# Optimization experiments

Hardware: AMD Instinct MI355X
Metric: run time of the kernel (lower is better)

Reference implementation:

```python
import jax, jax.numpy as jnp
import numpy as np
import math

N_NODES = 50000
N_EDGES = 600000
EMBED_DIM = 128


def setup_inputs() -> dict:
    key = jax.random.key(0)
    k_emb, k_edge, k_w = jax.random.split(key, 3)
    emb = jax.random.normal(k_emb, (N_NODES, EMBED_DIM), dtype=jnp.float32) * 0.1
    edges = jax.random.randint(k_edge, (2, N_EDGES), 0, N_NODES, dtype=jnp.int64)
    std = 1.0 / math.sqrt(EMBED_DIM)
    # nn.Linear(2*embed_dim, embed_dim): weight [out, in]
    W = jax.random.uniform(k_w, (EMBED_DIM, 2 * EMBED_DIM), dtype=jnp.float32,
                           minval=-std, maxval=std)
    b = jnp.zeros((EMBED_DIM,), dtype=jnp.float32)
    gamma = jnp.ones((EMBED_DIM,), dtype=jnp.float32)
    beta = jnp.zeros((EMBED_DIM,), dtype=jnp.float32)
    return {"emb": emb, "edges": edges, "W": W, "b": b, "gamma": gamma, "beta": beta}


def reference(emb, edges, W, b, gamma, beta):
    bsz = emb.shape[0]
    row = edges[0]  # destination / output node per edge (spmm row index)
    col = edges[1]  # source node per edge (spmm col index)
    # edge attention logits: <emb[dst], emb[src]> per edge, then exp
    attn = jnp.exp(jnp.sum(emb[row] * emb[col], axis=-1))  # [E]
    # special_spmm with ones -> per-row sum of attention weights
    denom = jax.ops.segment_sum(attn, row, num_segments=bsz)  # [N]
    # special_spmm with emb -> exp-weighted scatter-add of source embeddings
    agg = jax.ops.segment_sum(attn[:, None] * emb[col], row, num_segments=bsz)  # [N, D]
    agg = agg / (denom[:, None] + 1e-20)
    # concat + linear
    x = jnp.concatenate([emb, agg], axis=-1) @ W.T + b  # [N, D]
    # layer norm (eps=1e-5, affine)
    mu = jnp.mean(x, axis=-1, keepdims=True)
    var = jnp.mean((x - mu) ** 2, axis=-1, keepdims=True)
    x = (x - mu) * jax.lax.rsqrt(var + 1e-5) * gamma + beta
    return x
```

## Files before the change

kernel.cpp:

```cpp
#include <hip/hip_runtime.h>
#include <math.h>

#define D 128
#define TWO_D 256
#define CAP 64
#define CCAP 3584
#define CHUNK 2048

typedef __bf16 v8bf __attribute__((ext_vector_type(8)));
typedef float  v4f  __attribute__((ext_vector_type(4)));
typedef unsigned short us4 __attribute__((ext_vector_type(4)));
typedef unsigned short v8us __attribute__((ext_vector_type(8)));

#define OFF_CNT      0u
#define OFF_COLBUF   200192u
#define OFF_CCNT     6600192u
#define OFF_COARSE   6601216u
#define OFF_WBF16    10271232u
#define OFF_EMBB     10336768u
#define WS_TIER_A    23136768u

__global__ __launch_bounds__(256) void k_cvt_bin(
    const float* __restrict__ emb, const float* __restrict__ W,
    const int* __restrict__ edges,
    __bf16* __restrict__ embb, __bf16* __restrict__ Wb,
    unsigned int* __restrict__ ccnt, unsigned int* __restrict__ coarse,
    int nEmb8, int nW8, int E, int binB, int NB)
{
    if ((int)blockIdx.x < binB) {
        __shared__ unsigned int hist[256];
        __shared__ unsigned int base[256];
        __shared__ unsigned int run[256];
        int tid = threadIdx.x;
        int e0  = blockIdx.x * CHUNK;
        hist[tid] = 0;
        run[tid]  = 0;
        __syncthreads();

        int rs[CHUNK / 256];
        #pragma unroll
        for (int k = 0; k < CHUNK / 256; ++k) {
            int e = e0 + k * 256 + tid;
            rs[k] = -1;
            if (e < E) {
                int r = edges[e];
                rs[k] = r;
                atomicAdd(&hist[r >> 8], 1u);
            }
        }
        __syncthreads();
        if (tid < NB) {
            unsigned h = hist[tid];
            base[tid] = h ? atomicAdd(&ccnt[tid], h) : 0u;
        }
        __syncthreads();
        #pragma unroll
        for (int k = 0; k < CHUNK / 256; ++k) {
            int e = e0 + k * 256 + tid;
            if (e < E) {
                int r = rs[k];
                int c = edges[E + e];
                int bk = r >> 8;
                unsigned lp = atomicAdd(&run[bk], 1u);
                unsigned slot = base[bk] + lp;
                if (slot < CCAP)
                    coarse[(size_t)bk * CCAP + slot] =
                        ((unsigned)(r & 255) << 16) | (unsigned)c;
            }
        }
    } else {
        int tid = ((int)blockIdx.x - binB) * 256 + threadIdx.x;
        if (tid < nEmb8 + nW8) {
            const float* src;
            __bf16* dst;
            if (tid < nEmb8) { src = emb + (size_t)tid * 8; dst = embb + (size_t)tid * 8; }
            else { int j = (tid - nEmb8) * 8; src = W + j; dst = Wb + j; }
            float4 f0 = *(const float4*)(src);
            float4 f1 = *(const float4*)(src + 4);
            v8bf v;
            v[0] = (__bf16)f0.x; v[1] = (__bf16)f0.y; v[2] = (__bf16)f0.z; v[3] = (__bf16)f0.w;
            v[4] = (__bf16)f1.x; v[5] = (__bf16)f1.y; v[6] = (__bf16)f1.z; v[7] = (__bf16)f1.w;
            *(v8bf*)dst = v;
        }
    }
}

__global__ __launch_bounds__(256) void k_fine(
    const unsigned int* __restrict__ coarse,
    const unsigned int* __restrict__ ccnt,
    int* __restrict__ cnt, unsigned short* __restrict__ colbuf, int N)
{
    __shared__ __align__(16) unsigned short ftile[256 * CAP];
    __shared__ unsigned int fcnt[256];
    int tid = threadIdx.x;
    int b   = blockIdx.x;
    int r0  = b << 8;
    fcnt[tid] = 0;
    __syncthreads();

    unsigned mc = ccnt[b];
    if (mc > CCAP) mc = CCAP;
    for (unsigned i = tid; i < mc; i += 256) {
        unsigned p = coarse[(size_t)b * CCAP + i];
        unsigned rlo = p >> 16;
        unsigned c   = p & 0xFFFFu;
        unsigned lp  = atomicAdd(&fcnt[rlo], 1u);
        if (lp < CAP) ftile[rlo * CAP + lp] = (unsigned short)c;
    }
    __syncthreads();

    int r = r0 + tid;
    if (r < N) {
        unsigned d = fcnt[tid];
        cnt[r] = (int)(d > CAP ? CAP : d);
    }
    #pragma unroll
    for (int j = 0; j < 8; ++j) {
        int g  = j * 256 + tid;
        int rr = r0 + (g >> 3);
        if (rr < N)
            *(v8us*)(colbuf + (size_t)rr * CAP + (g & 7) * 8) =
                *(const v8us*)(ftile + (g >> 3) * CAP + (g & 7) * 8);
    }
}

__global__ __launch_bounds__(256) void gcn_agg_b(
    const __bf16* __restrict__ embb,
    const unsigned short* __restrict__ colbuf,
    const int* __restrict__ cnt,
    __bf16* __restrict__ aggb,
    int N)
{
    int grp = threadIdx.x >> 4;
    int il  = threadIdx.x & 15;
    int n   = blockIdx.x * 16 + grp;
    if (n >= N) return;

    v8bf a8 = *(const v8bf*)(embb + (size_t)n * D + il * 8);
    float af[8];
    #pragma unroll
    for (int q = 0; q < 8; ++q) af[q] = (float)a8[q];

    float acc[8];
    #pragma unroll
    for (int q = 0; q < 8; ++q) acc[q] = 0.f;
    float den = 0.f;

    int deg = cnt[n];
    if (deg > CAP) deg = CAP;
    const unsigned short* row = colbuf + (size_t)n * CAP;

    int e = 0;
    for (; e + 3 < deg; e += 4) {
        us4 c4 = *(const us4*)(row + e);
        v8bf v0 = *(const v8bf*)(embb + (size_t)c4[0] * D + il * 8);
        v8bf v1 = *(const v8bf*)(embb + (size_t)c4[1] * D + il * 8);
        v8bf v2 = *(const v8bf*)(embb + (size_t)c4[2] * D + il * 8);
        v8bf v3 = *(const v8bf*)(embb + (size_t)c4[3] * D + il * 8);
        float vf0[8], vf1[8], vf2[8], vf3[8];
        float t0 = 0.f, t1 = 0.f, t2 = 0.f, t3 = 0.f;
        #pragma unroll
        for (int q = 0; q < 8; ++q) {
            vf0[q] = (float)v0[q]; t0 += af[q] * vf0[q];
            vf1[q] = (float)v1[q]; t1 += af[q] * vf1[q];
            vf2[q] = (float)v2[q]; t2 += af[q] * vf2[q];
            vf3[q] = (float)v3[q]; t3 += af[q] * vf3[q];
        }
        #pragma unroll
        for (int off = 1; off <= 8; off <<= 1) {
            t0 += __shfl_xor(t0, off, 16);
            t1 += __shfl_xor(t1, off, 16);
            t2 += __shfl_xor(t2, off, 16);
            t3 += __shfl_xor(t3, off, 16);
        }
        float w0 = __expf(t0), w1 = __expf(t1);
        float w2 = __expf(t2), w3 = __expf(t3);
        #pragma unroll
        for (int q = 0; q < 8; ++q)
            acc[q] += (w0 * vf0[q] + w1 * vf1[q]) + (w2 * vf2[q] + w3 * vf3[q]);
        den += (w0 + w1) + (w2 + w3);
    }
    for (; e < deg; ++e) {
        int c0 = row[e];
        v8bf v0 = *(const v8bf*)(embb + (size_t)c0 * D + il * 8);
        float vf0[8];
        float t0 = 0.f;
        #pragma unroll
        for (int q = 0; q < 8; ++q) {
            vf0[q] = (float)v0[q];
            t0 += af[q] * vf0[q];
        }
        #pragma unroll
        for (int off = 1; off <= 8; off <<= 1)
            t0 += __shfl_xor(t0, off, 16);
        float w0 = __expf(t0);
        #pragma unroll
        for (int q = 0; q < 8; ++q) acc[q] += w0 * vf0[q];
        den += w0;
    }
    float inv = 1.0f / (den + 1e-20f);
    v8bf r;
    #pragma unroll
    for (int q = 0; q < 8; ++q) r[q] = (__bf16)(acc[q] * inv);
    *(v8bf*)(aggb + (size_t)n * 256 + il * 8) = r;
}

__global__ __launch_bounds__(256) void gcn_node_b(
    const __bf16* __restrict__ embb,
    const __bf16* __restrict__ Wb,
    const float* __restrict__ bias,
    const float* __restrict__ gamma,
    const float* __restrict__ beta,
    float* __restrict__ out, int N)
{
    __shared__ __align__(16) __bf16 xt[64 * 256];

    int t    = threadIdx.x;
    int wave = t >> 6;
    int lane = t & 63;
    int n0   = blockIdx.x * 64;
    const __bf16* aggb = (const __bf16*)out;

    #pragma unroll
    for (int j = 0; j < 8; ++j) {
        int gf = j * 64 + lane;
        int ml = gf >> 5;
        int m  = wave * 16 + ml;
        int g  = gf & 31;
        int n  = n0 + m;
        v8bf v;
        if (n < N) {
            v = (g < 16) ? *(const v8bf*)(embb + (size_t)n * D + g * 8)
                         : *(const v8bf*)(aggb + (size_t)n * 256 + (g - 16) * 8);
        } else {
            #pragma unroll
            for (int q = 0; q < 8; ++q) v[q] = (__bf16)0.0f;
        }
        *(v8bf*)(xt + (m * 32 + (g ^ (m & 7))) * 8) = v;
    }

    int mrow = lane & 15;
    int quad = lane >> 4;
    int mloc = wave * 16 + mrow;

    v8bf a[8];
    #pragma unroll
    for (int kt = 0; kt < 8; ++kt) {
        int g = (kt * 4 + quad) ^ (mloc & 7);
        a[kt] = *(const v8bf*)(xt + (mloc * 32 + g) * 8);
    }

    float bi[8], gm[8], bt[8];
    #pragma unroll
    for (int ft = 0; ft < 8; ++ft) {
        int f = ft * 16 + mrow;
        bi[ft] = bias[f]; gm[ft] = gamma[f]; bt[ft] = beta[f];
    }

    v4f accf[8];
    #pragma unroll
    for (int ft = 0; ft < 8; ++ft)
        #pragma unroll
        for (int r = 0; r < 4; ++r) accf[ft][r] = 0.0f;

    #pragma unroll
    for (int kt = 0; kt < 8; ++kt) {
        #pragma unroll
        for (int ft = 0; ft < 8; ++ft) {
            v8bf b = *(const v8bf*)(Wb + (ft * 16 + mrow) * TWO_D + kt * 32 + quad * 8);
            accf[ft] = __builtin_amdgcn_mfma_f32_16x16x32_bf16(a[kt], b, accf[ft], 0, 0, 0);
        }
    }

    #pragma unroll
    for (int ft = 0; ft < 8; ++ft)
        #pragma unroll
        for (int r = 0; r < 4; ++r) accf[ft][r] += bi[ft];

    #pragma unroll
    for (int r = 0; r < 4; ++r) {
        float s = 0.f, s2 = 0.f;
        #pragma unroll
        for (int ft = 0; ft < 8; ++ft) {
            float x = accf[ft][r];
            s += x; s2 += x * x;
        }
        #pragma unroll
        for (int off = 1; off <= 8; off <<= 1) {
            s  += __shfl_xor(s,  off, 64);
            s2 += __shfl_xor(s2, off, 64);
        }
        float mu  = s * (1.0f / 128.0f);
        float var = s2 * (1.0f / 128.0f) - mu * mu;
        float ivn = rsqrtf(var + 1e-5f);
        int n = n0 + wave * 16 + quad * 4 + r;
        if (n < N) {
            #pragma unroll
            for (int ft = 0; ft < 8; ++ft) {
                int f = ft * 16 + mrow;
                out[(size_t)n * D + f] = (accf[ft][r] - mu) * ivn * gm[ft] + bt[ft];
            }
        }
    }
}

__global__ __launch_bounds__(256) void gcn_edge_attn(
    const float* __restrict__ emb, const int* __restrict__ edges,
    float* __restrict__ agg, float* __restrict__ denom, int E) {
    int e    = (int)((blockIdx.x * 256u + threadIdx.x) >> 6);
    int lane = threadIdx.x & 63;
    if (e >= E) return;
    int row = edges[e];
    int col = edges[E + e];
    const float2 a = *(const float2*)(emb + (size_t)row * D + lane * 2);
    const float2 c = *(const float2*)(emb + (size_t)col * D + lane * 2);
    float s = a.x * c.x + a.y * c.y;
    #pragma unroll
    for (int off = 32; off >= 1; off >>= 1) s += __shfl_xor(s, off, 64);
    float attn = expf(s);
    float* dst = agg + (size_t)row * D + lane * 2;
    unsafeAtomicAdd(dst,     attn * c.x);
    unsafeAtomicAdd(dst + 1, attn * c.y);
    if (lane == 0) unsafeAtomicAdd(denom + row, attn);
}

__global__ __launch_bounds__(256) void gcn_node_fallback(
    const float* __restrict__ emb, const float* __restrict__ W,
    const float* __restrict__ bias, const float* __restrict__ gamma,
    const float* __restrict__ beta, const float* __restrict__ denom,
    float* __restrict__ out, int N) {
    __shared__ float scat[2][TWO_D];
    __shared__ float sred[2][4];
    int tid  = threadIdx.x;
    int g    = tid >> 7;
    int o    = tid & 127;
    int lane = tid & 63;
    int wig  = (tid >> 6) & 1;
    for (int n0 = blockIdx.x * 2; n0 < N; n0 += gridDim.x * 2) {
        int n = n0 + g;
        bool act = (n < N);
        if (act) {
            float ev  = emb[(size_t)n * D + o];
            float inv = 1.0f / (denom[n] + 1e-20f);
            scat[g][o]     = ev;
            scat[g][D + o] = out[(size_t)n * D + o] * inv;
        }
        __syncthreads();
        float acc = 0.f;
        if (act) {
            const float4* wr = (const float4*)(W + (size_t)o * TWO_D);
            #pragma unroll 4
            for (int k4 = 0; k4 < TWO_D / 4; ++k4) {
                float4 w = wr[k4];
                float4 a = *(const float4*)(&scat[g][k4 * 4]);
                acc += w.x * a.x + w.y * a.y + w.z * a.z + w.w * a.w;
            }
            acc += bias[o];
        }
        float s = acc, s2 = acc * acc;
        #pragma unroll
        for (int off = 32; off >= 1; off >>= 1) {
            s  += __shfl_xor(s,  off, 64);
            s2 += __shfl_xor(s2, off, 64);
        }
        if (lane == 0) { sred[g][wig * 2] = s; sred[g][wig * 2 + 1] = s2; }
        __syncthreads();
        if (act) {
            float ts  = sred[g][0] + sred[g][2];
            float ts2 = sred[g][1] + sred[g][3];
            float mu  = ts * (1.0f / 128.0f);
            float var = ts2 * (1.0f / 128.0f) - mu * mu;
            float inv = rsqrtf(var + 1e-5f);
            out[(size_t)n * D + o] = (acc - mu) * inv * gamma[o] + beta[o];
        }
        __syncthreads();
    }
}

extern "C" void kernel_launch(void* const* d_in, const int* in_sizes, int n_in,
                              void* d_out, int out_size, void* d_ws, size_t ws_size,
                              hipStream_t stream) {
    const float* emb   = (const float*)d_in[0];
    const int*   edges = (const int*)  d_in[1];
    const float* W     = (const float*)d_in[2];
    const float* bias  = (const float*)d_in[3];
    const float* gamma = (const float*)d_in[4];
    const float* beta  = (const float*)d_in[5];
    float* out = (float*)d_out;

    int N = in_sizes[0] / D;
    int E = in_sizes[1] / 2;

    if (ws_size >= (size_t)WS_TIER_A) {
        char* ws = (char*)d_ws;
        int*            cnt    = (int*)            (ws + OFF_CNT);
        unsigned short* colbuf = (unsigned short*) (ws + OFF_COLBUF);
        unsigned int*   ccnt   = (unsigned int*)   (ws + OFF_CCNT);
        unsigned int*   coarse = (unsigned int*)   (ws + OFF_COARSE);
        __bf16*         Wb     = (__bf16*)         (ws + OFF_WBF16);
        __bf16*         embb   = (__bf16*)         (ws + OFF_EMBB);

        int nEmb8 = N * D / 8;
        int nW8   = D * TWO_D / 8;
        int cvtB  = (nEmb8 + nW8 + 255) / 256;
        int binB  = (E + CHUNK - 1) / CHUNK;
        int NB    = (N + 255) >> 8;

        hipMemsetAsync(ccnt, 0, 1024, stream);
        k_cvt_bin<<<binB + cvtB, 256, 0, stream>>>(
            emb, W, edges, embb, Wb, ccnt, coarse, nEmb8, nW8, E, binB, NB);
        k_fine   <<<NB, 256, 0, stream>>>(coarse, ccnt, cnt, colbuf, N);
        gcn_agg_b<<<(N + 15) / 16, 256, 0, stream>>>(embb, colbuf, cnt,
                                                     (__bf16*)out, N);
        gcn_node_b<<<(N + 63) / 64, 256, 0, stream>>>(embb, Wb, bias, gamma,
                                                      beta, out, N);
    } else {
        float* denom = (float*)d_ws;
        hipMemsetAsync(out,   0, (size_t)N * D * sizeof(float), stream);
        hipMemsetAsync(denom, 0, (size_t)N * sizeof(float), stream);
        gcn_edge_attn<<<(E + 3) / 4, 256, 0, stream>>>(emb, edges, out, denom, E);
        gcn_node_fallback<<<512, 256, 0, stream>>>(emb, W, bias, gamma, beta,
                                                   denom, out, N);
    }
}
```

Measured before the change: 170.2 us.

## Unroll gather loop to 8 edges and streamline binning pass

The aggregation loop now handles 8 neighbours per iteration, issuing eight embedding-row gathers before any use to raise memory-level parallelism, with a 4-edge and a scalar tail. The binning kernel packs each edge's local offset into the histogram atomic's return value, which removes the second shared-memory atomic pass and the run array. CHUNK doubles to 4096, so fewer blocks do the binning. The 8-way unroll raises register pressure and may lower occupancy, and the 12-bit packed offset relies on CHUNK staying at or below 4096.

```diff
diff --git a/kernel.cpp b/kernel.cpp
--- a/kernel.cpp
+++ b/kernel.cpp
@@ -5,7 +5,7 @@
 #define TWO_D 256
 #define CAP 64
 #define CCAP 3584
-#define CHUNK 2048
+#define CHUNK 4096
 
 typedef __bf16 v8bf __attribute__((ext_vector_type(8)));
 typedef float  v4f  __attribute__((ext_vector_type(4)));
@@ -30,22 +30,19 @@
     if ((int)blockIdx.x < binB) {
         __shared__ unsigned int hist[256];
         __shared__ unsigned int base[256];
-        __shared__ unsigned int run[256];
         int tid = threadIdx.x;
         int e0  = blockIdx.x * CHUNK;
         hist[tid] = 0;
-        run[tid]  = 0;
-        __syncthreads();
-
-        int rs[CHUNK / 256];
+        __syncthreads();
+
+        unsigned rs[CHUNK / 256];
         #pragma unroll
         for (int k = 0; k < CHUNK / 256; ++k) {
             int e = e0 + k * 256 + tid;
-            rs[k] = -1;
             if (e < E) {
-                int r = edges[e];
-                rs[k] = r;
-                atomicAdd(&hist[r >> 8], 1u);
+                unsigned r  = (unsigned)edges[e];
+                unsigned lp = atomicAdd(&hist[r >> 8], 1u);
+                rs[k] = (r << 12) | lp;
             }
         }
         __syncthreads();
@@ -58,14 +55,14 @@
         for (int k = 0; k < CHUNK / 256; ++k) {
             int e = e0 + k * 256 + tid;
             if (e < E) {
-                int r = rs[k];
-                int c = edges[E + e];
+                unsigned pk = rs[k];
+                unsigned r  = pk >> 12;
+                unsigned lp = pk & 0xFFFu;
+                unsigned c  = (unsigned)edges[E + e];
                 int bk = r >> 8;
-                unsigned lp = atomicAdd(&run[bk], 1u);
                 unsigned slot = base[bk] + lp;
                 if (slot < CCAP)
-                    coarse[(size_t)bk * CCAP + slot] =
-                        ((unsigned)(r & 255) << 16) | (unsigned)c;
+                    coarse[(size_t)bk * CCAP + slot] = ((r & 255u) << 16) | c;
             }
         }
     } else {
@@ -151,20 +148,28 @@
     const unsigned short* row = colbuf + (size_t)n * CAP;
 
     int e = 0;
-    for (; e + 3 < deg; e += 4) {
-        us4 c4 = *(const us4*)(row + e);
-        v8bf v0 = *(const v8bf*)(embb + (size_t)c4[0] * D + il * 8);
-        v8bf v1 = *(const v8bf*)(embb + (size_t)c4[1] * D + il * 8);
-        v8bf v2 = *(const v8bf*)(embb + (size_t)c4[2] * D + il * 8);
-        v8bf v3 = *(const v8bf*)(embb + (size_t)c4[3] * D + il * 8);
-        float vf0[8], vf1[8], vf2[8], vf3[8];
+    for (; e + 7 < deg; e += 8) {
+        v8us c8 = *(const v8us*)(row + e);
+        v8bf r0 = *(const v8bf*)(embb + (size_t)c8[0] * D + il * 8);
+        v8bf r1 = *(const v8bf*)(embb + (size_t)c8[1] * D + il * 8);
+        v8bf r2 = *(const v8bf*)(embb + (size_t)c8[2] * D + il * 8);
+        v8bf r3 = *(const v8bf*)(embb + (size_t)c8[3] * D + il * 8);
+        v8bf r4 = *(const v8bf*)(embb + (size_t)c8[4] * D + il * 8);
+        v8bf r5 = *(const v8bf*)(embb + (size_t)c8[5] * D + il * 8);
+        v8bf r6 = *(const v8bf*)(embb + (size_t)c8[6] * D + il * 8);
+        v8bf r7 = *(const v8bf*)(embb + (size_t)c8[7] * D + il * 8);
         float t0 = 0.f, t1 = 0.f, t2 = 0.f, t3 = 0.f;
+        float t4 = 0.f, t5 = 0.f, t6 = 0.f, t7 = 0.f;
         #pragma unroll
         for (int q = 0; q < 8; ++q) {
-            vf0[q] = (float)v0[q]; t0 += af[q] * vf0[q];
-            vf1[q] = (float)v1[q]; t1 += af[q] * vf1[q];
-            vf2[q] = (float)v2[q]; t2 += af[q] * vf2[q];
-            vf3[q] = (float)v3[q]; t3 += af[q] * vf3[q];
+            t0 += af[q] * (float)r0[q];
+            t1 += af[q] * (float)r1[q];
+            t2 += af[q] * (float)r2[q];
+            t3 += af[q] * (float)r3[q];
+            t4 += af[q] * (float)r4[q];
+            t5 += af[q] * (float)r5[q];
+            t6 += af[q] * (float)r6[q];
+            t7 += af[q] * (float)r7[q];
         }
         #pragma unroll
         for (int off = 1; off <= 8; off <<= 1) {
@@ -172,30 +177,65 @@
             t1 += __shfl_xor(t1, off, 16);
             t2 += __shfl_xor(t2, off, 16);
             t3 += __shfl_xor(t3, off, 16);
+            t4 += __shfl_xor(t4, off, 16);
+            t5 += __shfl_xor(t5, off, 16);
+            t6 += __shfl_xor(t6, off, 16);
+            t7 += __shfl_xor(t7, off, 16);
         }
         float w0 = __expf(t0), w1 = __expf(t1);
         float w2 = __expf(t2), w3 = __expf(t3);
+        float w4 = __expf(t4), w5 = __expf(t5);
+        float w6 = __expf(t6), w7 = __expf(t7);
+        #pragma unroll
+        for (int q = 0; q < 8; ++q) {
+            acc[q] += (w0 * (float)r0[q] + w1 * (float)r1[q])
+                    + (w2 * (float)r2[q] + w3 * (float)r3[q])
+                    + (w4 * (float)r4[q] + w5 * (float)r5[q])
+                    + (w6 * (float)r6[q] + w7 * (float)r7[q]);
+        }
+        den += ((w0 + w1) + (w2 + w3)) + ((w4 + w5) + (w6 + w7));
+    }
+    for (; e + 3 < deg; e += 4) {
+        us4 c4 = *(const us4*)(row + e);
+        v8bf r0 = *(const v8bf*)(embb + (size_t)c4[0] * D + il * 8);
+        v8bf r1 = *(const v8bf*)(embb + (size_t)c4[1] * D + il * 8);
+        v8bf r2 = *(const v8bf*)(embb + (size_t)c4[2] * D + il * 8);
+        v8bf r3 = *(const v8bf*)(embb + (size_t)c4[3] * D + il * 8);
+        float t0 = 0.f, t1 = 0.f, t2 = 0.f, t3 = 0.f;
+        #pragma unroll
+        for (int q = 0; q < 8; ++q) {
+            t0 += af[q] * (float)r0[q];
+            t1 += af[q] * (float)r1[q];
+            t2 += af[q] * (float)r2[q];
+            t3 += af[q] * (float)r3[q];
+        }
+        #pragma unroll
+        for (int off = 1; off <= 8; off <<= 1) {
+            t0 += __shfl_xor(t0, off, 16);
+            t1 += __shfl_xor(t1, off, 16);
+            t2 += __shfl_xor(t2, off, 16);
+            t3 += __shfl_xor(t3, off, 16);
+        }
+        float w0 = __expf(t0), w1 = __expf(t1);
+        float w2 = __expf(t2), w3 = __expf(t3);
         #pragma unroll
         for (int q = 0; q < 8; ++q)
-            acc[q] += (w0 * vf0[q] + w1 * vf1[q]) + (w2 * vf2[q] + w3 * vf3[q]);
+            acc[q] += (w0 * (float)r0[q] + w1 * (float)r1[q])
+                    + (w2 * (float)r2[q] + w3 * (float)r3[q]);
         den += (w0 + w1) + (w2 + w3);
     }
     for (; e < deg; ++e) {
         int c0 = row[e];
-        v8bf v0 = *(const v8bf*)(embb + (size_t)c0 * D + il * 8);
-        float vf0[8];
+        v8bf r0 = *(const v8bf*)(embb + (size_t)c0 * D + il * 8);
         float t0 = 0.f;
         #pragma unroll
-        for (int q = 0; q < 8; ++q) {
-            vf0[q] = (float)v0[q];
-            t0 += af[q] * vf0[q];
-        }
+        for (int q = 0; q < 8; ++q) t0 += af[q] * (float)r0[q];
         #pragma unroll
         for (int off = 1; off <= 8; off <<= 1)
             t0 += __shfl_xor(t0, off, 16);
         float w0 = __expf(t0);
         #pragma unroll
-        for (int q = 0; q < 8; ++q) acc[q] += w0 * vf0[q];
+        for (int q = 0; q < 8; ++q) acc[q] += w0 * (float)r0[q];
         den += w0;
     }
     float inv = 1.0f / (den + 1e-20f);
```

After: 179.6 us. 5.5% more time.

## Assign one wavefront per node in aggregation and fuse binning slot atomics

Applied to the files above, without the earlier changes.

The aggregation kernel now gives each node a full 64-lane wavefront instead of a 16-lane group. Four 16-lane slots each process interleaved edges, and the partial sums are combined with cross-slot shuffles at the end, which spreads each node's gather latency over more lanes and shortens the per-thread serial edge loop. The binning kernel reuses the return value of the histogram atomic as the local slot, packing it with the row into a register. This drops the second shared-memory atomic pass and the run array. The costs are four times as many blocks and extra shuffle reductions, and the slot order within a bin may differ from before.

```diff
diff --git a/kernel.cpp b/kernel.cpp
--- a/kernel.cpp
+++ b/kernel.cpp
@@ -30,22 +30,19 @@
     if ((int)blockIdx.x < binB) {
         __shared__ unsigned int hist[256];
         __shared__ unsigned int base[256];
-        __shared__ unsigned int run[256];
         int tid = threadIdx.x;
         int e0  = blockIdx.x * CHUNK;
         hist[tid] = 0;
-        run[tid]  = 0;
-        __syncthreads();
-
-        int rs[CHUNK / 256];
+        __syncthreads();
+
+        unsigned rs[CHUNK / 256];
         #pragma unroll
         for (int k = 0; k < CHUNK / 256; ++k) {
             int e = e0 + k * 256 + tid;
-            rs[k] = -1;
             if (e < E) {
-                int r = edges[e];
-                rs[k] = r;
-                atomicAdd(&hist[r >> 8], 1u);
+                unsigned r  = (unsigned)edges[e];
+                unsigned lp = atomicAdd(&hist[r >> 8], 1u);
+                rs[k] = (r << 12) | lp;
             }
         }
         __syncthreads();
@@ -58,14 +55,14 @@
         for (int k = 0; k < CHUNK / 256; ++k) {
             int e = e0 + k * 256 + tid;
             if (e < E) {
-                int r = rs[k];
-                int c = edges[E + e];
+                unsigned pk = rs[k];
+                unsigned r  = pk >> 12;
+                unsigned lp = pk & 0xFFFu;
+                unsigned c  = (unsigned)edges[E + e];
                 int bk = r >> 8;
-                unsigned lp = atomicAdd(&run[bk], 1u);
                 unsigned slot = base[bk] + lp;
                 if (slot < CCAP)
-                    coarse[(size_t)bk * CCAP + slot] =
-                        ((unsigned)(r & 255) << 16) | (unsigned)c;
+                    coarse[(size_t)bk * CCAP + slot] = ((r & 255u) << 16) | c;
             }
         }
     } else {
@@ -131,9 +128,11 @@
     __bf16* __restrict__ aggb,
     int N)
 {
-    int grp = threadIdx.x >> 4;
-    int il  = threadIdx.x & 15;
-    int n   = blockIdx.x * 16 + grp;
+    int wid  = threadIdx.x >> 6;
+    int lane = threadIdx.x & 63;
+    int il   = lane & 15;
+    int slot = lane >> 4;
+    int n    = blockIdx.x * 4 + wid;
     if (n >= N) return;
 
     v8bf a8 = *(const v8bf*)(embb + (size_t)n * D + il * 8);
@@ -151,58 +150,74 @@
     const unsigned short* row = colbuf + (size_t)n * CAP;
 
     int e = 0;
-    for (; e + 3 < deg; e += 4) {
-        us4 c4 = *(const us4*)(row + e);
-        v8bf v0 = *(const v8bf*)(embb + (size_t)c4[0] * D + il * 8);
-        v8bf v1 = *(const v8bf*)(embb + (size_t)c4[1] * D + il * 8);
-        v8bf v2 = *(const v8bf*)(embb + (size_t)c4[2] * D + il * 8);
-        v8bf v3 = *(const v8bf*)(embb + (size_t)c4[3] * D + il * 8);
-        float vf0[8], vf1[8], vf2[8], vf3[8];
-        float t0 = 0.f, t1 = 0.f, t2 = 0.f, t3 = 0.f;
+    for (; e + 7 < deg; e += 8) {
+        v8us c8 = *(const v8us*)(row + e);
+        int ia = c8[slot];
+        int ib = c8[slot + 4];
+        v8bf ra = *(const v8bf*)(embb + (size_t)ia * D + il * 8);
+        v8bf rb = *(const v8bf*)(embb + (size_t)ib * D + il * 8);
+        float ta = 0.f, tb = 0.f;
         #pragma unroll
         for (int q = 0; q < 8; ++q) {
-            vf0[q] = (float)v0[q]; t0 += af[q] * vf0[q];
-            vf1[q] = (float)v1[q]; t1 += af[q] * vf1[q];
-            vf2[q] = (float)v2[q]; t2 += af[q] * vf2[q];
-            vf3[q] = (float)v3[q]; t3 += af[q] * vf3[q];
+            ta += af[q] * (float)ra[q];
+            tb += af[q] * (float)rb[q];
         }
         #pragma unroll
         for (int off = 1; off <= 8; off <<= 1) {
-            t0 += __shfl_xor(t0, off, 16);
-            t1 += __shfl_xor(t1, off, 16);
-            t2 += __shfl_xor(t2, off, 16);
-            t3 += __shfl_xor(t3, off, 16);
-        }
-        float w0 = __expf(t0), w1 = __expf(t1);
-        float w2 = __expf(t2), w3 = __expf(t3);
+            ta += __shfl_xor(ta, off, 16);
+            tb += __shfl_xor(tb, off, 16);
+        }
+        float wa = __expf(ta), wb = __expf(tb);
         #pragma unroll
         for (int q = 0; q < 8; ++q)
-            acc[q] += (w0 * vf0[q] + w1 * vf1[q]) + (w2 * vf2[q] + w3 * vf3[q]);
-        den += (w0 + w1) + (w2 + w3);
-    }
-    for (; e < deg; ++e) {
-        int c0 = row[e];
-        v8bf v0 = *(const v8bf*)(embb + (size_t)c0 * D + il * 8);
-        float vf0[8];
-        float t0 = 0.f;
-        #pragma unroll
-        for (int q = 0; q < 8; ++q) {
-            vf0[q] = (float)v0[q];
-            t0 += af[q] * vf0[q];
-        }
-        #pragma unroll
-        for (int off = 1; off <= 8; off <<= 1)
-            t0 += __shfl_xor(t0, off, 16);
-        float w0 = __expf(t0);
-        #pragma unroll
-        for (int q = 0; q < 8; ++q) acc[q] += w0 * vf0[q];
-        den += w0;
-    }
-    float inv = 1.0f / (den + 1e-20f);
-    v8bf r;
-    #pragma unroll
-    for (int q = 0; q < 8; ++q) r[q] = (__bf16)(acc[q] * inv);
-    *(v8bf*)(aggb + (size_t)n * 256 + il * 8) = r;
+            acc[q] += wa * (float)ra[q] + wb * (float)rb[q];
+        den += wa + wb;
+    }
+    int rem = deg - e;
+    if (rem > 0) {
+        v8us c8 = *(const v8us*)(row + e);
+        if (slot < rem) {
+            int ia = c8[slot];
+            v8bf ra = *(const v8bf*)(embb + (size_t)ia * D + il * 8);
+            float ta = 0.f;
+            #pragma unroll
+            for (int q = 0; q < 8; ++q) ta += af[q] * (float)ra[q];
+            #pragma unroll
+            for (int off = 1; off <= 8; off <<= 1) ta += __shfl_xor(ta, off, 16);
+            float wa = __expf(ta);
+            #pragma unroll
+            for (int q = 0; q < 8; ++q) acc[q] += wa * (float)ra[q];
+            den += wa;
+        }
+        if (slot + 4 < rem) {
+            int ib = c8[slot + 4];
+            v8bf rb = *(const v8bf*)(embb + (size_t)ib * D + il * 8);
+            float tb = 0.f;
+            #pragma unroll
+            for (int q = 0; q < 8; ++q) tb += af[q] * (float)rb[q];
+            #pragma unroll
+            for (int off = 1; off <= 8; off <<= 1) tb += __shfl_xor(tb, off, 16);
+            float wb = __expf(tb);
+            #pragma unroll
+            for (int q = 0; q < 8; ++q) acc[q] += wb * (float)rb[q];
+            den += wb;
+        }
+    }
+    #pragma unroll
+    for (int q = 0; q < 8; ++q) {
+        acc[q] += __shfl_xor(acc[q], 16, 64);
+        acc[q] += __shfl_xor(acc[q], 32, 64);
+    }
+    den += __shfl_xor(den, 16, 64);
+    den += __shfl_xor(den, 32, 64);
+
+    if (slot == 0) {
+        float inv = 1.0f / (den + 1e-20f);
+        v8bf r;
+        #pragma unroll
+        for (int q = 0; q < 8; ++q) r[q] = (__bf16)(acc[q] * inv);
+        *(v8bf*)(aggb + (size_t)n * 256 + il * 8) = r;
+    }
 }
 
 __global__ __launch_bounds__(256) void gcn_node_b(
@@ -410,8 +425,8 @@
         k_cvt_bin<<<binB + cvtB, 256, 0, stream>>>(
             emb, W, edges, embb, Wb, ccnt, coarse, nEmb8, nW8, E, binB, NB);
         k_fine   <<<NB, 256, 0, stream>>>(coarse, ccnt, cnt, colbuf, N);
-        gcn_agg_b<<<(N + 15) / 16, 256, 0, stream>>>(embb, colbuf, cnt,
-                                                     (__bf16*)out, N);
+        gcn_agg_b<<<(N + 3) / 4, 256, 0, stream>>>(embb, colbuf, cnt,
+                                                   (__bf16*)out, N);
         gcn_node_b<<<(N + 63) / 64, 256, 0, stream>>>(embb, Wb, bias, gamma,
                                                       beta, out, N);
     } else {
```

Result: no change. 171.8 us (+0.9%).
